# Kernel tuning notes

Hardware: AMD Instinct MI355X
Metric: run time of the kernel (lower is better)

## Reference

```python
import jax, jax.numpy as jnp
import numpy as np
import math

B, T, L = 32, 512, 128
IN_C, D, H, NL = 512, 512, 8, 6
HD = D // H
DFF = 2 * D  # dim_feedforward = hidden_dim * 2 per __init__
V = 8000
BASE = 10000.0
EPS = 1e-5


def _rope_tables(n, hd):
    # standard RoPE: half-dim frequencies duplicated, matching precompute_rope_sin_cos
    inv = 1.0 / (BASE ** (jnp.arange(0, hd, 2, dtype=jnp.float32) / hd))
    ang = jnp.arange(n, dtype=jnp.float32)[:, None] * inv[None, :]  # [n, hd/2]
    cos = jnp.concatenate([jnp.cos(ang), jnp.cos(ang)], axis=-1)    # [n, hd]
    sin = jnp.concatenate([jnp.sin(ang), jnp.sin(ang)], axis=-1)
    return cos, sin


def _rot_half(x):
    x1, x2 = jnp.split(x, 2, axis=-1)
    return jnp.concatenate([-x2, x1], axis=-1)


def _ln(x, g, b):
    m = x.mean(-1, keepdims=True)
    v = jnp.mean((x - m) ** 2, axis=-1, keepdims=True)
    return (x - m) / jnp.sqrt(v + EPS) * g + b


def setup_inputs() -> dict:
    key = jax.random.key(0)
    ks = jax.random.split(key, 24)
    w = lambda k, s: jax.random.normal(k, s, jnp.float32) * 0.02
    z = lambda s: jnp.zeros(s, jnp.float32)
    o = lambda s: jnp.ones(s, jnp.float32)
    return {
        'encoder_features': jax.random.normal(ks[0], (B, T, IN_C), jnp.float32),
        'targets': jax.random.randint(ks[1], (B, L), 0, V),
        'emb': w(ks[2], (V, D)),
        'inp_w': w(ks[3], (D, IN_C)), 'inp_b': z((D,)),
        'out_w': w(ks[4], (V, D)), 'out_b': z((V,)),
        'qw': w(ks[5], (D, D)), 'qb': z((D,)),
        'kw': w(ks[6], (D, D)), 'kb': z((D,)),
        'vw': w(ks[7], (D, D)), 'vb': z((D,)),
        'ow': w(ks[8], (D, D)), 'ob': z((D,)),
        'mha_w': w(ks[9], (3 * D, D)), 'mha_b': z((3 * D,)),
        'mha_ow': w(ks[10], (D, D)), 'mha_ob': z((D,)),
        'w1': w(ks[11], (DFF, D)), 'b1': z((DFF,)),
        'w2': w(ks[12], (D, DFF)), 'b2': z((D,)),
        'ln1_g': o((D,)), 'ln1_b': z((D,)),
        'ln2_g': o((D,)), 'ln2_b': z((D,)),
        'ln3_g': o((D,)), 'ln3_b': z((D,)),
    }


def reference(encoder_features, targets, emb, inp_w, inp_b, out_w, out_b,
              qw, qb, kw, kb, vw, vb, ow, ob, mha_w, mha_b, mha_ow, mha_ob,
              w1, b1, w2, b2, ln1_g, ln1_b, ln2_g, ln2_b, ln3_g, ln3_b):
    memory = encoder_features @ inp_w.T + inp_b               # [B,T,D]
    tgt = emb[targets] * math.sqrt(D)                          # [B,L,D]
    mem_pad = jnp.abs(memory).sum(-1) == 0                     # [B,T] key padding mask
    causal = jnp.tril(jnp.ones((L, L), dtype=bool))
    cos, sin = _rope_tables(L, HD)                             # pos_ids = arange(0, L)
    scale = 1.0 / math.sqrt(HD)
    wq, wk, wv = jnp.split(mha_w, 3, axis=0)
    bq, bk, bv = jnp.split(mha_b, 3)

    for _ in range(NL):  # all layers share the same weights (ModuleList of one object)
        # --- self-attention with RoPE ---
        q = (tgt @ qw.T + qb).reshape(B, L, H, HD).transpose(0, 2, 1, 3)
        k = (tgt @ kw.T + kb).reshape(B, L, H, HD).transpose(0, 2, 1, 3)
        v = (tgt @ vw.T + vb).reshape(B, L, H, HD).transpose(0, 2, 1, 3)
        q = q * cos + _rot_half(q) * sin
        k = k * cos + _rot_half(k) * sin
        s = jnp.einsum('bhqd,bhkd->bhqk', q, k) * scale
        s = jnp.where(causal, s, -jnp.inf)
        a = jax.nn.softmax(s, axis=-1)
        o_sa = jnp.einsum('bhqk,bhkd->bhqd', a, v).transpose(0, 2, 1, 3).reshape(B, L, D)
        tgt = _ln(tgt + o_sa @ ow.T + ob, ln1_g, ln1_b)
        # --- cross-attention (nn.MultiheadAttention, batch_first) ---
        q2 = (tgt @ wq.T + bq).reshape(B, L, H, HD).transpose(0, 2, 1, 3)
        k2 = (memory @ wk.T + bk).reshape(B, T, H, HD).transpose(0, 2, 1, 3)
        v2 = (memory @ wv.T + bv).reshape(B, T, H, HD).transpose(0, 2, 1, 3)
        s2 = jnp.einsum('bhqd,bhkd->bhqk', q2, k2) * scale
        s2 = jnp.where(mem_pad[:, None, None, :], -jnp.inf, s2)
        a2 = jax.nn.softmax(s2, axis=-1)
        o_ca = jnp.einsum('bhqk,bhkd->bhqd', a2, v2).transpose(0, 2, 1, 3).reshape(B, L, D)
        tgt = _ln(tgt + o_ca @ mha_ow.T + mha_ob, ln2_g, ln2_b)
        # --- FFN (exact GELU, as nn.GELU default) ---
        ff = jax.nn.gelu(tgt @ w1.T + b1, approximate=False) @ w2.T + b2
        tgt = _ln(tgt + ff, ln3_g, ln3_b)

    logits = tgt @ out_w.T + out_b  # [B,L,V]
    return logits, tgt
```

## Files before the change

kernel.cpp:

```cpp
#include <hip/hip_runtime.h>
#include <hip/hip_bf16.h>

#define B_ 32
#define T_ 512
#define L_ 128
#define INC_ 512
#define D_ 512
#define H_ 8
#define HD_ 64
#define NL_ 6
#define DFF_ 1024
#define V_ 8000
#define LDSK 40
#define AST 72

typedef __bf16 bfr;
typedef __attribute__((ext_vector_type(8))) __bf16 bf16x8;
typedef __attribute__((ext_vector_type(4))) __bf16 bf16x4;
typedef __attribute__((ext_vector_type(4))) float f32x4;

struct ConvDesc { const float* src; bfr* dst; int n; int blk0; };
struct ConvTable { ConvDesc e[12]; int ne; };

__global__ void conv_many_kernel(ConvTable tab)
{
    int b = blockIdx.x;
    for (int i = 0; i < tab.ne; ++i) {
        const ConvDesc d = tab.e[i];
        int nb = (d.n + 255) >> 8;
        if (b >= d.blk0 && b < d.blk0 + nb) {
            int g = (b - d.blk0) * 256 + threadIdx.x;
            if (g < d.n) d.dst[g] = (bfr)d.src[g];
            return;
        }
    }
}

__global__ void copy3_kernel(const float* a, const float* b, const float* c, float* dst)
{
    int g = blockIdx.x * 256 + threadIdx.x;
    if (g < D_) dst[g] = a[g];
    else if (g < 2 * D_) dst[g] = b[g - D_];
    else if (g < 3 * D_) dst[g] = c[g - 2 * D_];
}

__device__ __forceinline__ void tile_map(int bid, int nbm, int nbn, int& pm, int& pn)
{
    int nwg = nbm * nbn;
    int q = nwg >> 3, r = nwg & 7;
    int xcd = bid & 7, idx = bid >> 3;
    int wgid = (xcd < r ? xcd * (q + 1) : r * (q + 1) + (xcd - r) * q) + idx;
    const int GROUP = 8;
    int per_group = GROUP * nbn;
    int gid = wgid / per_group;
    int first = gid * GROUP;
    int gsz = min(nbm - first, GROUP);
    int rem = wgid - gid * per_group;
    pm = first + rem % gsz;
    pn = rem / gsz;
}

template <int OUT>
__global__ __launch_bounds__(256) void gemm_split(
    const float* __restrict__ A, const bfr* __restrict__ Whi,
    const float* __restrict__ bias, float* __restrict__ Cf, bfr* __restrict__ Cb,
    int M, int N, int K)
{
    __shared__ bfr Ah_s[128 * LDSK];
    __shared__ bfr Wh_s[64 * LDSK];
    const int t = threadIdx.x;
    const int bm = blockIdx.y * 128, bn = blockIdx.x * 64;
    const int w = t >> 6, lane = t & 63;
    const int wm = w >> 1, wn = w & 1;
    const int fr = lane & 15, kq = lane >> 4;
    const int ar = t >> 1, ah = (t & 1) * 16;
    const int wr = t >> 2, wk = (t & 3) * 8;

    f32x4 acc[4][2] = {};

    for (int k0 = 0; k0 < K; k0 += 32) {
        {
            const float* ap = A + (size_t)(bm + ar) * K + (k0 + ah);
            float4 v0 = ((const float4*)ap)[0];
            float4 v1 = ((const float4*)ap)[1];
            float4 v2 = ((const float4*)ap)[2];
            float4 v3 = ((const float4*)ap)[3];
            float xs[16] = {v0.x, v0.y, v0.z, v0.w, v1.x, v1.y, v1.z, v1.w,
                            v2.x, v2.y, v2.z, v2.w, v3.x, v3.y, v3.z, v3.w};
            bf16x8 h0, h1;
#pragma unroll
            for (int i = 0; i < 8; ++i) h0[i] = (bfr)xs[i];
#pragma unroll
            for (int i = 0; i < 8; ++i) h1[i] = (bfr)xs[8 + i];
            *(bf16x8*)(Ah_s + ar * LDSK + ah) = h0;
            *(bf16x8*)(Ah_s + ar * LDSK + ah + 8) = h1;
        }
        *(bf16x8*)(Wh_s + wr * LDSK + wk) = *(const bf16x8*)(Whi + (size_t)(bn + wr) * K + (k0 + wk));
        __syncthreads();
        bf16x8 Afh[4], Wfh[2];
#pragma unroll
        for (int i = 0; i < 4; ++i)
            Afh[i] = *(const bf16x8*)(Ah_s + (wm * 64 + i * 16 + fr) * LDSK + kq * 8);
#pragma unroll
        for (int j = 0; j < 2; ++j)
            Wfh[j] = *(const bf16x8*)(Wh_s + (wn * 32 + j * 16 + fr) * LDSK + kq * 8);
#pragma unroll
        for (int i = 0; i < 4; ++i)
#pragma unroll
            for (int j = 0; j < 2; ++j)
                acc[i][j] = __builtin_amdgcn_mfma_f32_16x16x32_bf16(Afh[i], Wfh[j], acc[i][j], 0, 0, 0);
        __syncthreads();
    }
#pragma unroll
    for (int i = 0; i < 4; ++i) {
        int row0 = bm + wm * 64 + i * 16 + (lane >> 4) * 4;
#pragma unroll
        for (int j = 0; j < 2; ++j) {
            int col = bn + wn * 32 + j * 16 + fr;
            float bj = bias[col];
#pragma unroll
            for (int r = 0; r < 4; ++r) {
                float v = acc[i][j][r] + bj;
                if (OUT == 0) Cf[(size_t)(row0 + r) * N + col] = v;
                else Cb[(size_t)(row0 + r) * N + col] = (bfr)v;
            }
        }
    }
}

template <int ACT, int OUT, int BM>
__global__ __launch_bounds__(256, 2) void gemm_ps(
    const bfr* __restrict__ Ahi,
    const bfr* __restrict__ Whi,
    const float* __restrict__ bias, float* __restrict__ Cf,
    bfr* __restrict__ Chi, int M, int N, int K)
{
    constexpr int MF = BM / 32;
    __shared__ bfr Ah_s[BM * LDSK];
    __shared__ bfr Wh_s[64 * LDSK];
    const int t = threadIdx.x;
    int pm, pn;
    tile_map(blockIdx.x, M / BM, N / 64, pm, pn);
    const int bm = pm * BM, bn = pn * 64;
    const int w = t >> 6, lane = t & 63;
    const int wm = w >> 1, wn = w & 1;
    const int fr = lane & 15, kq = lane >> 4;
    const int wr = t >> 2, wk = (t & 3) * 8;

    f32x4 acc[MF][2] = {};

    for (int k0 = 0; k0 < K; k0 += 32) {
        if constexpr (BM == 128) {
            const int ar = t >> 1, ah = (t & 1) * 16;
            const bfr* ap = Ahi + (size_t)(bm + ar) * K + (k0 + ah);
            *(bf16x8*)(Ah_s + ar * LDSK + ah) = *(const bf16x8*)ap;
            *(bf16x8*)(Ah_s + ar * LDSK + ah + 8) = *(const bf16x8*)(ap + 8);
        } else {
            const int ar = t >> 2, ah = (t & 3) * 8;
            *(bf16x8*)(Ah_s + ar * LDSK + ah) = *(const bf16x8*)(Ahi + (size_t)(bm + ar) * K + (k0 + ah));
        }
        *(bf16x8*)(Wh_s + wr * LDSK + wk) = *(const bf16x8*)(Whi + (size_t)(bn + wr) * K + (k0 + wk));
        __syncthreads();
        bf16x8 Afh[MF], Wfh[2];
#pragma unroll
        for (int i = 0; i < MF; ++i)
            Afh[i] = *(const bf16x8*)(Ah_s + (wm * (BM / 2) + i * 16 + fr) * LDSK + kq * 8);
#pragma unroll
        for (int j = 0; j < 2; ++j)
            Wfh[j] = *(const bf16x8*)(Wh_s + (wn * 32 + j * 16 + fr) * LDSK + kq * 8);
#pragma unroll
        for (int i = 0; i < MF; ++i)
#pragma unroll
            for (int j = 0; j < 2; ++j)
                acc[i][j] = __builtin_amdgcn_mfma_f32_16x16x32_bf16(Afh[i], Wfh[j], acc[i][j], 0, 0, 0);
        __syncthreads();
    }
#pragma unroll
    for (int i = 0; i < MF; ++i) {
        int row0 = bm + wm * (BM / 2) + i * 16 + (lane >> 4) * 4;
#pragma unroll
        for (int j = 0; j < 2; ++j) {
            int col = bn + wn * 32 + j * 16 + fr;
            float bj = bias[col];
#pragma unroll
            for (int r = 0; r < 4; ++r) {
                float v = acc[i][j][r] + bj;
                if (ACT == 1) v = 0.5f * v * (1.0f + erff(v * 0.70710678118654752f));
                size_t idx = (size_t)(row0 + r) * N + col;
                if (OUT == 0) Cf[idx] = v;
                else Chi[idx] = (bfr)v;
            }
        }
    }
}

template <int TK, int CAUSAL>
__global__ __launch_bounds__(256) void attn_kernel(
    const bfr* __restrict__ Qg, int qstr,
    const bfr* __restrict__ Kg, const bfr* __restrict__ Vg, int kvstr,
    const int* __restrict__ pad,
    const float* __restrict__ cosT, const float* __restrict__ sinT,
    bfr* __restrict__ Ohi)
{
    __shared__ bfr Qs[64 * AST];
    __shared__ bfr Ks[64 * AST];
    __shared__ bfr VTs[64 * AST];
    __shared__ bfr Ps[64 * AST];
    const int bidx = blockIdx.x;
    const int qt = bidx & 1, bh = bidx >> 1;
    const int h = bh & 7, b = bh >> 3;
    const int t = threadIdx.x;
    const int w = t >> 6, lane = t & 63;
    const int l4 = lane & 15, hi4 = lane >> 4;
    const int q0 = qt * 64;
    const int srow = t >> 2, ht = t & 3;

    if (CAUSAL) {
        int qrow = q0 + srow;
        const bfr* qp = Qg + (size_t)(b * L_ + qrow) * qstr + h * HD_ + ht * 8;
        bf16x8 a = *(const bf16x8*)qp;
        bf16x8 bb = *(const bf16x8*)(qp + 32);
        bf16x8 o1, o2;
#pragma unroll
        for (int j = 0; j < 8; ++j) {
            float c = cosT[qrow * 32 + ht * 8 + j], s = sinT[qrow * 32 + ht * 8 + j];
            float x1 = (float)a[j], x2 = (float)bb[j];
            o1[j] = (bfr)(x1 * c - x2 * s);
            o2[j] = (bfr)(x2 * c + x1 * s);
        }
        *(bf16x8*)(Qs + srow * AST + ht * 8) = o1;
        *(bf16x8*)(Qs + srow * AST + ht * 8 + 32) = o2;
    } else {
        const bfr* qp = Qg + (size_t)(b * L_ + q0 + srow) * qstr + h * HD_ + ht * 16;
        *(bf16x8*)(Qs + srow * AST + ht * 16) = *(const bf16x8*)qp;
        *(bf16x8*)(Qs + srow * AST + ht * 16 + 8) = *(const bf16x8*)(qp + 8);
    }

    f32x4 o_acc[4] = {};
    float m_run[4], l_run[4];
#pragma unroll
    for (int r = 0; r < 4; ++r) { m_run[r] = -1e30f; l_run[r] = 0.f; }

    const int NT = CAUSAL ? (qt + 1) : (TK / 64);
    for (int kt = 0; kt < NT; ++kt) {
        __syncthreads();
        if (CAUSAL) {
            int krow = kt * 64 + srow;
            const bfr* kp = Kg + (size_t)(b * TK + krow) * kvstr + h * HD_ + ht * 8;
            bf16x8 a = *(const bf16x8*)kp;
            bf16x8 bb = *(const bf16x8*)(kp + 32);
            bf16x8 o1, o2;
#pragma unroll
            for (int j = 0; j < 8; ++j) {
                float c = cosT[krow * 32 + ht * 8 + j], s = sinT[krow * 32 + ht * 8 + j];
                float x1 = (float)a[j], x2 = (float)bb[j];
                o1[j] = (bfr)(x1 * c - x2 * s);
                o2[j] = (bfr)(x2 * c + x1 * s);
            }
            *(bf16x8*)(Ks + srow * AST + ht * 8) = o1;
            *(bf16x8*)(Ks + srow * AST + ht * 8 + 32) = o2;
        } else {
            const bfr* kp = Kg + (size_t)(b * TK + kt * 64 + srow) * kvstr + h * HD_ + ht * 16;
            *(bf16x8*)(Ks + srow * AST + ht * 16) = *(const bf16x8*)kp;
            *(bf16x8*)(Ks + srow * AST + ht * 16 + 8) = *(const bf16x8*)(kp + 8);
        }
        {
            const bfr* vp = Vg + (size_t)(b * TK + kt * 64 + srow) * kvstr + h * HD_ + ht * 16;
            bf16x8 v0 = *(const bf16x8*)vp;
            bf16x8 v1 = *(const bf16x8*)(vp + 8);
#pragma unroll
            for (int i = 0; i < 8; ++i) VTs[(ht * 16 + i) * AST + srow] = v0[i];
#pragma unroll
            for (int i = 0; i < 8; ++i) VTs[(ht * 16 + 8 + i) * AST + srow] = v1[i];
        }
        __syncthreads();

        f32x4 s[4] = {};
#pragma unroll
        for (int kk = 0; kk < 64; kk += 32) {
            bf16x8 a = *(const bf16x8*)(Qs + (w * 16 + l4) * AST + kk + hi4 * 8);
#pragma unroll
            for (int n = 0; n < 4; ++n) {
                bf16x8 bb = *(const bf16x8*)(Ks + (n * 16 + l4) * AST + kk + hi4 * 8);
                s[n] = __builtin_amdgcn_mfma_f32_16x16x32_bf16(a, bb, s[n], 0, 0, 0);
            }
        }
        float madd[4];
        if (!CAUSAL) {
#pragma unroll
            for (int n = 0; n < 4; ++n)
                madd[n] = pad[b * TK + kt * 64 + n * 16 + l4] ? -1e30f : 0.f;
        }
#pragma unroll
        for (int r = 0; r < 4; ++r) {
            int qrow = q0 + w * 16 + hi4 * 4 + r;
            float sv[4];
#pragma unroll
            for (int n = 0; n < 4; ++n) {
                float x = s[n][r] * 0.125f;
                if (CAUSAL) {
                    int col = kt * 64 + n * 16 + l4;
                    if (col > qrow) x = -1e30f;
                } else x += madd[n];
                sv[n] = x;
            }
            float mx = fmaxf(fmaxf(sv[0], sv[1]), fmaxf(sv[2], sv[3]));
#pragma unroll
            for (int off = 1; off < 16; off <<= 1) mx = fmaxf(mx, __shfl_xor(mx, off));
            float mnew = fmaxf(m_run[r], mx);
            float alpha = expf(m_run[r] - mnew);
            float pv[4], psum = 0.f;
#pragma unroll
            for (int n = 0; n < 4; ++n) { pv[n] = expf(sv[n] - mnew); psum += pv[n]; }
#pragma unroll
            for (int off = 1; off < 16; off <<= 1) psum += __shfl_xor(psum, off);
            l_run[r] = l_run[r] * alpha + psum;
            m_run[r] = mnew;
#pragma unroll
            for (int n = 0; n < 4; ++n) o_acc[n][r] *= alpha;
#pragma unroll
            for (int n = 0; n < 4; ++n)
                Ps[(w * 16 + hi4 * 4 + r) * AST + n * 16 + l4] = (bfr)pv[n];
        }
#pragma unroll
        for (int kk = 0; kk < 64; kk += 32) {
            bf16x8 pa = *(const bf16x8*)(Ps + (w * 16 + l4) * AST + kk + hi4 * 8);
#pragma unroll
            for (int n = 0; n < 4; ++n) {
                bf16x8 vb = *(const bf16x8*)(VTs + (n * 16 + l4) * AST + kk + hi4 * 8);
                o_acc[n] = __builtin_amdgcn_mfma_f32_16x16x32_bf16(pa, vb, o_acc[n], 0, 0, 0);
            }
        }
    }
#pragma unroll
    for (int r = 0; r < 4; ++r) {
        float inv = 1.0f / l_run[r];
        int qrow = q0 + w * 16 + hi4 * 4 + r;
#pragma unroll
        for (int n = 0; n < 4; ++n)
            Ohi[(size_t)(b * L_ + qrow) * D_ + h * HD_ + n * 16 + l4] = (bfr)(o_acc[n][r] * inv);
    }
}

__global__ void rope_tables_kernel(float* __restrict__ cosT, float* __restrict__ sinT)
{
    int gid = blockIdx.x * blockDim.x + threadIdx.x;
    if (gid >= L_ * 32) return;
    int l = gid >> 5, i = gid & 31;
    float inv = powf(10000.0f, -(float)(2 * i) / (float)HD_);
    float ang = (float)l * inv;
    cosT[gid] = cosf(ang);
    sinT[gid] = sinf(ang);
}

__global__ void embed_kernel(const int* __restrict__ targets, const float* __restrict__ emb,
                             float* __restrict__ tgt, bfr* __restrict__ thi)
{
    int gid = blockIdx.x * blockDim.x + threadIdx.x;
    if (gid >= B_ * L_ * D_) return;
    int d = gid & (D_ - 1);
    int r = gid >> 9;
    int tok = targets[r];
    float x = emb[(size_t)tok * D_ + d] * 22.62741699796952f;
    tgt[gid] = x;
    thi[gid] = (bfr)x;
}

__global__ void pad_kernel(const float* __restrict__ mem, int* __restrict__ pad)
{
    int gid = blockIdx.x * blockDim.x + threadIdx.x;
    if (gid >= B_ * T_) return;
    const float* p = mem + (size_t)gid * D_;
    float s = 0.f;
    for (int d = 0; d < D_; ++d) s += fabsf(p[d]);
    pad[gid] = (s == 0.0f) ? 1 : 0;
}

__global__ __launch_bounds__(128) void ln_residual_kernel(
    const float* __restrict__ tgt, const float* __restrict__ delta,
    const float* __restrict__ g, const float* __restrict__ bb,
    float* __restrict__ yout, bfr* __restrict__ thi)
{
    const int row = blockIdx.x;
    const int t = threadIdx.x;
    __shared__ float rbuf[128];
    size_t base = (size_t)row * D_ + t * 4;
    float4 x = *(const float4*)(tgt + base);
    float4 dl = *(const float4*)(delta + base);
    x.x += dl.x; x.y += dl.y; x.z += dl.z; x.w += dl.w;
    rbuf[t] = x.x + x.y + x.z + x.w;
    __syncthreads();
    for (int off = 64; off > 0; off >>= 1) { if (t < off) rbuf[t] += rbuf[t + off]; __syncthreads(); }
    float mean = rbuf[0] * (1.0f / D_);
    __syncthreads();
    float4 d4 = {x.x - mean, x.y - mean, x.z - mean, x.w - mean};
    rbuf[t] = d4.x * d4.x + d4.y * d4.y + d4.z * d4.z + d4.w * d4.w;
    __syncthreads();
    for (int off = 64; off > 0; off >>= 1) { if (t < off) rbuf[t] += rbuf[t + off]; __syncthreads(); }
    float inv = 1.0f / sqrtf(rbuf[0] * (1.0f / D_) + 1e-5f);
    float4 g4 = *(const float4*)(g + t * 4);
    float4 b4 = *(const float4*)(bb + t * 4);
    float4 y = {d4.x * inv * g4.x + b4.x, d4.y * inv * g4.y + b4.y,
                d4.z * inv * g4.z + b4.z, d4.w * inv * g4.w + b4.w};
    *(float4*)(yout + base) = y;
    bf16x4 h4 = {(bfr)y.x, (bfr)y.y, (bfr)y.z, (bfr)y.w};
    *(bf16x4*)(thi + base) = h4;
}

__global__ void fillf_kernel(float* p, float v, size_t n)
{
    size_t gid = (size_t)blockIdx.x * 256 + threadIdx.x;
    if (gid < n) p[gid] = v;
}

extern "C" void kernel_launch(void* const* d_in, const int* in_sizes, int n_in,
                              void* d_out, int out_size, void* d_ws, size_t ws_size,
                              hipStream_t stream)
{
    const float* enc    = (const float*)d_in[0];
    const int*   tg     = (const int*)d_in[1];
    const float* emb    = (const float*)d_in[2];
    const float* inp_w  = (const float*)d_in[3];
    const float* inp_b  = (const float*)d_in[4];
    const float* out_w  = (const float*)d_in[5];
    const float* out_b  = (const float*)d_in[6];
    const float* qw     = (const float*)d_in[7];
    const float* qb     = (const float*)d_in[8];
    const float* kw     = (const float*)d_in[9];
    const float* kb     = (const float*)d_in[10];
    const float* vw     = (const float*)d_in[11];
    const float* vb     = (const float*)d_in[12];
    const float* ow     = (const float*)d_in[13];
    const float* ob     = (const float*)d_in[14];
    const float* mha_w  = (const float*)d_in[15];
    const float* mha_b  = (const float*)d_in[16];
    const float* mha_ow = (const float*)d_in[17];
    const float* mha_ob = (const float*)d_in[18];
    const float* w1     = (const float*)d_in[19];
    const float* b1     = (const float*)d_in[20];
    const float* w2     = (const float*)d_in[21];
    const float* b2     = (const float*)d_in[22];
    const float* ln1g   = (const float*)d_in[23];
    const float* ln1b   = (const float*)d_in[24];
    const float* ln2g   = (const float*)d_in[25];
    const float* ln2b   = (const float*)d_in[26];
    const float* ln3g   = (const float*)d_in[27];
    const float* ln3b   = (const float*)d_in[28];

    const int BL = B_ * L_;
    const int BT = B_ * T_;
    const size_t N_LOGITS = (size_t)BL * V_;
    const int D2 = D_ * D_;

    const size_t WS_NEEDED =
        (size_t)BT * 1024 * sizeof(bfr)
        + (size_t)BL * D_ * sizeof(float)
        + (size_t)BL * D_ * sizeof(bfr)
        + (size_t)2 * L_ * 32 * sizeof(float) + (size_t)BT * sizeof(int)
        + (size_t)V_ * D_ * sizeof(bfr);
    if (ws_size < WS_NEEDED) {
        fillf_kernel<<<((size_t)out_size + 255) / 256, 256, 0, stream>>>((float*)d_out, 0.f, (size_t)out_size);
        return;
    }
    bfr*   f_KVb = (bfr*)d_ws;
    float* f_tgt = (float*)(f_KVb + (size_t)BT * 1024);
    bfr*   tgt_hi = (bfr*)(f_tgt + (size_t)BL * D_);
    float* f_cos = (float*)(tgt_hi + (size_t)BL * D_);
    float* f_sin = f_cos + (size_t)L_ * 32;
    int*   f_pad = (int*)(f_sin + (size_t)L_ * 32);
    bfr*   ow_hi = (bfr*)(f_pad + BT);

    bfr* wp = (bfr*)d_out;
    bfr* qkvw_hi = wp;  wp += 3 * D2;
    bfr* inp_hi  = wp;  wp += D2;
    bfr* mha_hi  = wp;  wp += 3 * D2;
    bfr* o_hi    = wp;  wp += D2;
    bfr* mo_hi   = wp;  wp += D2;
    bfr* w1_hi   = wp;  wp += DFF_ * D_;
    bfr* w2_hi   = wp;  wp += D_ * DFF_;
    float* f_qkvb = (float*)wp;
    float* lr    = f_qkvb + 3 * D_;
    float* f_t2  = lr;
    bfr*   qkv   = (bfr*)(f_t2 + (size_t)BL * D_);
    bfr*   qcr   = qkv + (size_t)BL * 3 * D_;
    bfr*   t1_hi = qcr + (size_t)BL * D_;
    bfr*   ffh_hi = t1_hi + (size_t)BL * D_;
    float* f_mem = lr;

    {
        ConvTable tab{};
        int blk = 0, ne = 0;
        auto add = [&](const float* s, bfr* d, int n) {
            tab.e[ne] = {s, d, n, blk};
            blk += (n + 255) >> 8;
            ++ne;
        };
        add(qw, qkvw_hi, D2);
        add(kw, qkvw_hi + D2, D2);
        add(vw, qkvw_hi + 2 * D2, D2);
        add(inp_w, inp_hi, D2);
        add(mha_w, mha_hi, 3 * D2);
        add(ow, o_hi, D2);
        add(mha_ow, mo_hi, D2);
        add(w1, w1_hi, DFF_ * D_);
        add(w2, w2_hi, D_ * DFF_);
        add(out_w, ow_hi, V_ * D_);
        tab.ne = ne;
        conv_many_kernel<<<blk, 256, 0, stream>>>(tab);
    }
    copy3_kernel<<<6, 256, 0, stream>>>(qb, kb, vb, f_qkvb);

    rope_tables_kernel<<<(L_ * 32 + 255) / 256, 256, 0, stream>>>(f_cos, f_sin);
    embed_kernel<<<(BL * D_ + 255) / 256, 256, 0, stream>>>(tg, emb, f_tgt, tgt_hi);

    gemm_split<0><<<dim3(D_ / 64, BT / 128), 256, 0, stream>>>(enc, inp_hi, inp_b, f_mem, nullptr, BT, D_, INC_);
    pad_kernel<<<(BT + 255) / 256, 256, 0, stream>>>(f_mem, f_pad);
    gemm_split<1><<<dim3(1024 / 64, BT / 128), 256, 0, stream>>>(f_mem, mha_hi + (size_t)D2, mha_b + D_, nullptr, f_KVb, BT, 1024, D_);

    float* o_logits = (float*)d_out;
    float* o_tgt = o_logits + N_LOGITS;

    for (int layer = 0; layer < NL_; ++layer) {
        gemm_ps<0, 1, 64><<<(BL / 64) * (3 * D_ / 64), 256, 0, stream>>>(tgt_hi, qkvw_hi, f_qkvb, nullptr, qkv, BL, 3 * D_, D_);
        attn_kernel<L_, 1><<<B_ * H_ * 2, 256, 0, stream>>>(qkv, 3 * D_, qkv + D_, qkv + 2 * D_, 3 * D_, nullptr, f_cos, f_sin, t1_hi);
        gemm_ps<0, 0, 64><<<(BL / 64) * (D_ / 64), 256, 0, stream>>>(t1_hi, o_hi, ob, f_t2, nullptr, BL, D_, D_);
        ln_residual_kernel<<<BL, 128, 0, stream>>>(f_tgt, f_t2, ln1g, ln1b, f_tgt, tgt_hi);
        gemm_ps<0, 1, 64><<<(BL / 64) * (D_ / 64), 256, 0, stream>>>(tgt_hi, mha_hi, mha_b, nullptr, qcr, BL, D_, D_);
        attn_kernel<T_, 0><<<B_ * H_ * 2, 256, 0, stream>>>(qcr, D_, f_KVb, f_KVb + D_, 1024, f_pad, nullptr, nullptr, t1_hi);
        gemm_ps<0, 0, 64><<<(BL / 64) * (D_ / 64), 256, 0, stream>>>(t1_hi, mo_hi, mha_ob, f_t2, nullptr, BL, D_, D_);
        ln_residual_kernel<<<BL, 128, 0, stream>>>(f_tgt, f_t2, ln2g, ln2b, f_tgt, tgt_hi);
        gemm_ps<1, 1, 64><<<(BL / 64) * (DFF_ / 64), 256, 0, stream>>>(tgt_hi, w1_hi, b1, nullptr, ffh_hi, BL, DFF_, D_);
        gemm_ps<0, 0, 64><<<(BL / 64) * (D_ / 64), 256, 0, stream>>>(ffh_hi, w2_hi, b2, f_t2, nullptr, BL, D_, DFF_);
        float* yout = (layer == NL_ - 1) ? o_tgt : f_tgt;
        ln_residual_kernel<<<BL, 128, 0, stream>>>(f_tgt, f_t2, ln3g, ln3b, yout, tgt_hi);
    }

    gemm_ps<0, 0, 128><<<(BL / 128) * (V_ / 64), 256, 0, stream>>>(tgt_hi, ow_hi, out_b, o_logits, nullptr, BL, V_, D_);
}
```

Before: 1.095 ms.

## Merge attention query tiles into one wide block and use bf16 memory path

Attention kernels now use one 512-thread block per batch-head covering all 128 query rows, so each K/V tile is loaded once and shared instead of once per query half. The encoder features are converted to bf16 in the existing conversion kernel, and the memory projection and cross-attention KV GEMMs reuse the tiled gemm_ps kernel with bf16 output. This removes the float-input split GEMM and halves memory traffic for the encoder-side tensors. It gives up causal tile skipping and halves the number of attention blocks, and pad detection now reads rounded bf16 memory.

```diff
diff --git a/kernel.cpp b/kernel.cpp
--- a/kernel.cpp
+++ b/kernel.cpp
@@ -60,74 +60,6 @@
     pn = rem / gsz;
 }
 
-template <int OUT>
-__global__ __launch_bounds__(256) void gemm_split(
-    const float* __restrict__ A, const bfr* __restrict__ Whi,
-    const float* __restrict__ bias, float* __restrict__ Cf, bfr* __restrict__ Cb,
-    int M, int N, int K)
-{
-    __shared__ bfr Ah_s[128 * LDSK];
-    __shared__ bfr Wh_s[64 * LDSK];
-    const int t = threadIdx.x;
-    const int bm = blockIdx.y * 128, bn = blockIdx.x * 64;
-    const int w = t >> 6, lane = t & 63;
-    const int wm = w >> 1, wn = w & 1;
-    const int fr = lane & 15, kq = lane >> 4;
-    const int ar = t >> 1, ah = (t & 1) * 16;
-    const int wr = t >> 2, wk = (t & 3) * 8;
-
-    f32x4 acc[4][2] = {};
-
-    for (int k0 = 0; k0 < K; k0 += 32) {
-        {
-            const float* ap = A + (size_t)(bm + ar) * K + (k0 + ah);
-            float4 v0 = ((const float4*)ap)[0];
-            float4 v1 = ((const float4*)ap)[1];
-            float4 v2 = ((const float4*)ap)[2];
-            float4 v3 = ((const float4*)ap)[3];
-            float xs[16] = {v0.x, v0.y, v0.z, v0.w, v1.x, v1.y, v1.z, v1.w,
-                            v2.x, v2.y, v2.z, v2.w, v3.x, v3.y, v3.z, v3.w};
-            bf16x8 h0, h1;
-#pragma unroll
-            for (int i = 0; i < 8; ++i) h0[i] = (bfr)xs[i];
-#pragma unroll
-            for (int i = 0; i < 8; ++i) h1[i] = (bfr)xs[8 + i];
-            *(bf16x8*)(Ah_s + ar * LDSK + ah) = h0;
-            *(bf16x8*)(Ah_s + ar * LDSK + ah + 8) = h1;
-        }
-        *(bf16x8*)(Wh_s + wr * LDSK + wk) = *(const bf16x8*)(Whi + (size_t)(bn + wr) * K + (k0 + wk));
-        __syncthreads();
-        bf16x8 Afh[4], Wfh[2];
-#pragma unroll
-        for (int i = 0; i < 4; ++i)
-            Afh[i] = *(const bf16x8*)(Ah_s + (wm * 64 + i * 16 + fr) * LDSK + kq * 8);
-#pragma unroll
-        for (int j = 0; j < 2; ++j)
-            Wfh[j] = *(const bf16x8*)(Wh_s + (wn * 32 + j * 16 + fr) * LDSK + kq * 8);
-#pragma unroll
-        for (int i = 0; i < 4; ++i)
-#pragma unroll
-            for (int j = 0; j < 2; ++j)
-                acc[i][j] = __builtin_amdgcn_mfma_f32_16x16x32_bf16(Afh[i], Wfh[j], acc[i][j], 0, 0, 0);
-        __syncthreads();
-    }
-#pragma unroll
-    for (int i = 0; i < 4; ++i) {
-        int row0 = bm + wm * 64 + i * 16 + (lane >> 4) * 4;
-#pragma unroll
-        for (int j = 0; j < 2; ++j) {
-            int col = bn + wn * 32 + j * 16 + fr;
-            float bj = bias[col];
-#pragma unroll
-            for (int r = 0; r < 4; ++r) {
-                float v = acc[i][j][r] + bj;
-                if (OUT == 0) Cf[(size_t)(row0 + r) * N + col] = v;
-                else Cb[(size_t)(row0 + r) * N + col] = (bfr)v;
-            }
-        }
-    }
-}
-
 template <int ACT, int OUT, int BM>
 __global__ __launch_bounds__(256, 2) void gemm_ps(
     const bfr* __restrict__ Ahi,
@@ -195,76 +127,79 @@
 }
 
 template <int TK, int CAUSAL>
-__global__ __launch_bounds__(256) void attn_kernel(
+__global__ __launch_bounds__(512) void attn_wide(
     const bfr* __restrict__ Qg, int qstr,
     const bfr* __restrict__ Kg, const bfr* __restrict__ Vg, int kvstr,
     const int* __restrict__ pad,
     const float* __restrict__ cosT, const float* __restrict__ sinT,
     bfr* __restrict__ Ohi)
 {
-    __shared__ bfr Qs[64 * AST];
+    __shared__ bfr Qs[128 * AST];
     __shared__ bfr Ks[64 * AST];
     __shared__ bfr VTs[64 * AST];
-    __shared__ bfr Ps[64 * AST];
-    const int bidx = blockIdx.x;
-    const int qt = bidx & 1, bh = bidx >> 1;
+    __shared__ bfr Ps[128 * AST];
+    const int bh = blockIdx.x;
     const int h = bh & 7, b = bh >> 3;
     const int t = threadIdx.x;
     const int w = t >> 6, lane = t & 63;
     const int l4 = lane & 15, hi4 = lane >> 4;
-    const int q0 = qt * 64;
-    const int srow = t >> 2, ht = t & 3;
-
-    if (CAUSAL) {
-        int qrow = q0 + srow;
-        const bfr* qp = Qg + (size_t)(b * L_ + qrow) * qstr + h * HD_ + ht * 8;
-        bf16x8 a = *(const bf16x8*)qp;
-        bf16x8 bb = *(const bf16x8*)(qp + 32);
-        bf16x8 o1, o2;
-#pragma unroll
-        for (int j = 0; j < 8; ++j) {
-            float c = cosT[qrow * 32 + ht * 8 + j], s = sinT[qrow * 32 + ht * 8 + j];
-            float x1 = (float)a[j], x2 = (float)bb[j];
-            o1[j] = (bfr)(x1 * c - x2 * s);
-            o2[j] = (bfr)(x2 * c + x1 * s);
-        }
-        *(bf16x8*)(Qs + srow * AST + ht * 8) = o1;
-        *(bf16x8*)(Qs + srow * AST + ht * 8 + 32) = o2;
-    } else {
-        const bfr* qp = Qg + (size_t)(b * L_ + q0 + srow) * qstr + h * HD_ + ht * 16;
-        *(bf16x8*)(Qs + srow * AST + ht * 16) = *(const bf16x8*)qp;
-        *(bf16x8*)(Qs + srow * AST + ht * 16 + 8) = *(const bf16x8*)(qp + 8);
-    }
-
-    f32x4 o_acc[4] = {};
-    float m_run[4], l_run[4];
-#pragma unroll
-    for (int r = 0; r < 4; ++r) { m_run[r] = -1e30f; l_run[r] = 0.f; }
-
-    const int NT = CAUSAL ? (qt + 1) : (TK / 64);
-    for (int kt = 0; kt < NT; ++kt) {
-        __syncthreads();
+    const int qr0 = w * 16;
+
+    {
+        const int srow = t >> 2, ht = t & 3;
         if (CAUSAL) {
-            int krow = kt * 64 + srow;
-            const bfr* kp = Kg + (size_t)(b * TK + krow) * kvstr + h * HD_ + ht * 8;
-            bf16x8 a = *(const bf16x8*)kp;
-            bf16x8 bb = *(const bf16x8*)(kp + 32);
+            const bfr* qp = Qg + (size_t)(b * L_ + srow) * qstr + h * HD_ + ht * 8;
+            bf16x8 a = *(const bf16x8*)qp;
+            bf16x8 bb = *(const bf16x8*)(qp + 32);
             bf16x8 o1, o2;
 #pragma unroll
             for (int j = 0; j < 8; ++j) {
-                float c = cosT[krow * 32 + ht * 8 + j], s = sinT[krow * 32 + ht * 8 + j];
+                float c = cosT[srow * 32 + ht * 8 + j], s = sinT[srow * 32 + ht * 8 + j];
                 float x1 = (float)a[j], x2 = (float)bb[j];
                 o1[j] = (bfr)(x1 * c - x2 * s);
                 o2[j] = (bfr)(x2 * c + x1 * s);
             }
-            *(bf16x8*)(Ks + srow * AST + ht * 8) = o1;
-            *(bf16x8*)(Ks + srow * AST + ht * 8 + 32) = o2;
+            *(bf16x8*)(Qs + srow * AST + ht * 8) = o1;
+            *(bf16x8*)(Qs + srow * AST + ht * 8 + 32) = o2;
         } else {
-            const bfr* kp = Kg + (size_t)(b * TK + kt * 64 + srow) * kvstr + h * HD_ + ht * 16;
-            *(bf16x8*)(Ks + srow * AST + ht * 16) = *(const bf16x8*)kp;
-            *(bf16x8*)(Ks + srow * AST + ht * 16 + 8) = *(const bf16x8*)(kp + 8);
-        }
-        {
+            const bfr* qp = Qg + (size_t)(b * L_ + srow) * qstr + h * HD_ + ht * 16;
+            *(bf16x8*)(Qs + srow * AST + ht * 16) = *(const bf16x8*)qp;
+            *(bf16x8*)(Qs + srow * AST + ht * 16 + 8) = *(const bf16x8*)(qp + 8);
+        }
+    }
+
+    f32x4 o_acc[4] = {};
+    float m_run[4], l_run[4];
+#pragma unroll
+    for (int r = 0; r < 4; ++r) { m_run[r] = -1e30f; l_run[r] = 0.f; }
+
+    for (int kt = 0; kt < TK / 64; ++kt) {
+        __syncthreads();
+        if (t < 256) {
+            const int srow = t >> 2, ht = t & 3;
+            int krow = kt * 64 + srow;
+            if (CAUSAL) {
+                const bfr* kp = Kg + (size_t)(b * TK + krow) * kvstr + h * HD_ + ht * 8;
+                bf16x8 a = *(const bf16x8*)kp;
+                bf16x8 bb = *(const bf16x8*)(kp + 32);
+                bf16x8 o1, o2;
+#pragma unroll
+                for (int j = 0; j < 8; ++j) {
+                    float c = cosT[krow * 32 + ht * 8 + j], s = sinT[krow * 32 + ht * 8 + j];
+                    float x1 = (float)a[j], x2 = (float)bb[j];
+                    o1[j] = (bfr)(x1 * c - x2 * s);
+                    o2[j] = (bfr)(x2 * c + x1 * s);
+                }
+                *(bf16x8*)(Ks + srow * AST + ht * 8) = o1;
+                *(bf16x8*)(Ks + srow * AST + ht * 8 + 32) = o2;
+            } else {
+                const bfr* kp = Kg + (size_t)(b * TK + krow) * kvstr + h * HD_ + ht * 16;
+                *(bf16x8*)(Ks + srow * AST + ht * 16) = *(const bf16x8*)kp;
+                *(bf16x8*)(Ks + srow * AST + ht * 16 + 8) = *(const bf16x8*)(kp + 8);
+            }
+        } else {
+            const int tt = t - 256;
+            const int srow = tt >> 2, ht = tt & 3;
             const bfr* vp = Vg + (size_t)(b * TK + kt * 64 + srow) * kvstr + h * HD_ + ht * 16;
             bf16x8 v0 = *(const bf16x8*)vp;
             bf16x8 v1 = *(const bf16x8*)(vp + 8);
@@ -278,7 +213,7 @@
         f32x4 s[4] = {};
 #pragma unroll
         for (int kk = 0; kk < 64; kk += 32) {
-            bf16x8 a = *(const bf16x8*)(Qs + (w * 16 + l4) * AST + kk + hi4 * 8);
+            bf16x8 a = *(const bf16x8*)(Qs + (qr0 + l4) * AST + kk + hi4 * 8);
 #pragma unroll
             for (int n = 0; n < 4; ++n) {
                 bf16x8 bb = *(const bf16x8*)(Ks + (n * 16 + l4) * AST + kk + hi4 * 8);
@@ -293,7 +228,7 @@
         }
 #pragma unroll
         for (int r = 0; r < 4; ++r) {
-            int qrow = q0 + w * 16 + hi4 * 4 + r;
+            int qrow = qr0 + hi4 * 4 + r;
             float sv[4];
 #pragma unroll
             for (int n = 0; n < 4; ++n) {
@@ -320,11 +255,11 @@
             for (int n = 0; n < 4; ++n) o_acc[n][r] *= alpha;
 #pragma unroll
             for (int n = 0; n < 4; ++n)
-                Ps[(w * 16 + hi4 * 4 + r) * AST + n * 16 + l4] = (bfr)pv[n];
+                Ps[(qr0 + hi4 * 4 + r) * AST + n * 16 + l4] = (bfr)pv[n];
         }
 #pragma unroll
         for (int kk = 0; kk < 64; kk += 32) {
-            bf16x8 pa = *(const bf16x8*)(Ps + (w * 16 + l4) * AST + kk + hi4 * 8);
+            bf16x8 pa = *(const bf16x8*)(Ps + (qr0 + l4) * AST + kk + hi4 * 8);
 #pragma unroll
             for (int n = 0; n < 4; ++n) {
                 bf16x8 vb = *(const bf16x8*)(VTs + (n * 16 + l4) * AST + kk + hi4 * 8);
@@ -335,7 +270,7 @@
 #pragma unroll
     for (int r = 0; r < 4; ++r) {
         float inv = 1.0f / l_run[r];
-        int qrow = q0 + w * 16 + hi4 * 4 + r;
+        int qrow = qr0 + hi4 * 4 + r;
 #pragma unroll
         for (int n = 0; n < 4; ++n)
             Ohi[(size_t)(b * L_ + qrow) * D_ + h * HD_ + n * 16 + l4] = (bfr)(o_acc[n][r] * inv);
@@ -366,13 +301,17 @@
     thi[gid] = (bfr)x;
 }
 
-__global__ void pad_kernel(const float* __restrict__ mem, int* __restrict__ pad)
+__global__ void pad_kernel(const bfr* __restrict__ mem, int* __restrict__ pad)
 {
     int gid = blockIdx.x * blockDim.x + threadIdx.x;
     if (gid >= B_ * T_) return;
-    const float* p = mem + (size_t)gid * D_;
+    const bfr* p = mem + (size_t)gid * D_;
     float s = 0.f;
-    for (int d = 0; d < D_; ++d) s += fabsf(p[d]);
+    for (int d0 = 0; d0 < D_; d0 += 8) {
+        bf16x8 v = *(const bf16x8*)(p + d0);
+#pragma unroll
+        for (int j = 0; j < 8; ++j) s += fabsf((float)v[j]);
+    }
     pad[gid] = (s == 0.0f) ? 1 : 0;
 }
 
@@ -485,7 +424,8 @@
     bfr*   qcr   = qkv + (size_t)BL * 3 * D_;
     bfr*   t1_hi = qcr + (size_t)BL * D_;
     bfr*   ffh_hi = t1_hi + (size_t)BL * D_;
-    float* f_mem = lr;
+    bfr*   enc_hi = (bfr*)lr;
+    bfr*   mem_hi = enc_hi + (size_t)BT * D_;
 
     {
         ConvTable tab{};
@@ -505,6 +445,7 @@
         add(w1, w1_hi, DFF_ * D_);
         add(w2, w2_hi, D_ * DFF_);
         add(out_w, ow_hi, V_ * D_);
+        add(enc, enc_hi, BT * D_);
         tab.ne = ne;
         conv_many_kernel<<<blk, 256, 0, stream>>>(tab);
     }
@@ -513,20 +454,20 @@
     rope_tables_kernel<<<(L_ * 32 + 255) / 256, 256, 0, stream>>>(f_cos, f_sin);
     embed_kernel<<<(BL * D_ + 255) / 256, 256, 0, stream>>>(tg, emb, f_tgt, tgt_hi);
 
-    gemm_split<0><<<dim3(D_ / 64, BT / 128), 256, 0, stream>>>(enc, inp_hi, inp_b, f_mem, nullptr, BT, D_, INC_);
-    pad_kernel<<<(BT + 255) / 256, 256, 0, stream>>>(f_mem, f_pad);
-    gemm_split<1><<<dim3(1024 / 64, BT / 128), 256, 0, stream>>>(f_mem, mha_hi + (size_t)D2, mha_b + D_, nullptr, f_KVb, BT, 1024, D_);
+    gemm_ps<0, 1, 128><<<(BT / 128) * (D_ / 64), 256, 0, stream>>>(enc_hi, inp_hi, inp_b, nullptr, mem_hi, BT, D_, INC_);
+    pad_kernel<<<(BT + 255) / 256, 256, 0, stream>>>(mem_hi, f_pad);
+    gemm_ps<0, 1, 128><<<(BT / 128) * (1024 / 64), 256, 0, stream>>>(mem_hi, mha_hi + (size_t)D2, mha_b + D_, nullptr, f_KVb, BT, 1024, D_);
 
     float* o_logits = (float*)d_out;
     float* o_tgt = o_logits + N_LOGITS;
 
     for (int layer = 0; layer < NL_; ++layer) {
         gemm_ps<0, 1, 64><<<(BL / 64) * (3 * D_ / 64), 256, 0, stream>>>(tgt_hi, qkvw_hi, f_qkvb, nullptr, qkv, BL, 3 * D_, D_);
-        attn_kernel<L_, 1><<<B_ * H_ * 2, 256, 0, stream>>>(qkv, 3 * D_, qkv + D_, qkv + 2 * D_, 3 * D_, nullptr, f_cos, f_sin, t1_hi);
+        attn_wide<L_, 1><<<B_ * H_, 512, 0, stream>>>(qkv, 3 * D_, qkv + D_, qkv + 2 * D_, 3 * D_, nullptr, f_cos, f_sin, t1_hi);
         gemm_ps<0, 0, 64><<<(BL / 64) * (D_ / 64), 256, 0, stream>>>(t1_hi, o_hi, ob, f_t2, nullptr, BL, D_, D_);
         ln_residual_kernel<<<BL, 128, 0, stream>>>(f_tgt, f_t2, ln1g, ln1b, f_tgt, tgt_hi);
         gemm_ps<0, 1, 64><<<(BL / 64) * (D_ / 64), 256, 0, stream>>>(tgt_hi, mha_hi, mha_b, nullptr, qcr, BL, D_, D_);
-        attn_kernel<T_, 0><<<B_ * H_ * 2, 256, 0, stream>>>(qcr, D_, f_KVb, f_KVb + D_, 1024, f_pad, nullptr, nullptr, t1_hi);
+        attn_wide<T_, 0><<<B_ * H_, 512, 0, stream>>>(qcr, D_, f_KVb, f_KVb + D_, 1024, f_pad, nullptr, nullptr, t1_hi);
         gemm_ps<0, 0, 64><<<(BL / 64) * (D_ / 64), 256, 0, stream>>>(t1_hi, mo_hi, mha_ob, f_t2, nullptr, BL, D_, D_);
         ln_residual_kernel<<<BL, 128, 0, stream>>>(f_tgt, f_t2, ln2g, ln2b, f_tgt, tgt_hi);
         gemm_ps<1, 1, 64><<<(BL / 64) * (DFF_ / 64), 256, 0, stream>>>(tgt_hi, w1_hi, b1, nullptr, ffh_hi, BL, DFF_, D_);
```

After: 1.041 ms. 1.05x faster.
